# Optimization experiments

Measured on AMD Instinct MI355X. Metric: run time of the kernel, lower is better.

Reference implementation:

```python
import jax, jax.numpy as jnp
import numpy as np

NEG_INF = -9e15  # matches torch's -9000000000000000.0 fill
ALPHA = 0.2      # LeakyReLU negative slope


def setup_inputs() -> dict:
    key = jax.random.key(0)
    k1, k2, k3, k4 = jax.random.split(key, 4)
    B, F, N, T, C = 16, 128, 256, 64, 64
    h = jax.random.normal(k1, (B, F, N, T), dtype=jnp.float32)
    adj = jax.random.randint(k2, (B, N, N), 0, 2, dtype=jnp.int32)
    W = jax.random.normal(k3, (B, F, C), dtype=jnp.float32)
    a = jax.random.normal(k4, (B, 2 * C, 1), dtype=jnp.float32)
    return {"h": h, "adj": adj, "W": W, "a": a}


def reference(h, adj, W, a):
    # Wh: (B, C, N, T)
    Wh = jnp.einsum('bfnt,bfc->bcnt', h, W)
    C = W.shape[-1]
    # The original builds the O(N^2) pairwise concat then contracts with a.
    # Equivalently: e[b,i,j,t] = leakyrelu(a1.Wh[:, i] + a2.Wh[:, j])
    a1 = a[:, :C, 0]   # (B, C)
    a2 = a[:, C:, 0]   # (B, C)
    f = jnp.einsum('bcnt,bc->bnt', Wh, a1)  # (B, N, T)
    g = jnp.einsum('bcnt,bc->bnt', Wh, a2)  # (B, N, T)
    e = jax.nn.leaky_relu(f[:, :, None, :] + g[:, None, :, :], negative_slope=ALPHA)  # (B,N,N,T)
    mask = adj[:, :, :, None] > 0  # (B, N, N, 1) broadcast over T
    e = jnp.where(mask, e, NEG_INF)
    attention = jax.nn.softmax(e, axis=2)  # softmax over neighbor index m
    # dropout = 0.0 (eval-mode reference), so skipped
    h_prime = jnp.einsum('bnmt,bcmt->bcnt', attention, Wh)
    return jax.nn.elu(h_prime)  # concat=True branch
```

## Files before the change

### kernel.cpp

```cpp
#include <hip/hip_runtime.h>

#define B_ 16
#define F_ 128
#define N_ 256
#define T_ 64
#define C_ 64
#define ALPHA_ 0.2f
#define L2E_ 1.4426950408889634f

typedef short bf16x8 __attribute__((ext_vector_type(8)));
typedef float f32x4 __attribute__((ext_vector_type(4)));

__device__ __forceinline__ unsigned short f2bf(float x){
  unsigned int u = __float_as_uint(x);
  unsigned int r = u + 0x7FFFu + ((u >> 16) & 1u);
  return (unsigned short)(r >> 16);
}
__device__ __forceinline__ unsigned pk2(float a, float b){
  return ((unsigned)f2bf(b) << 16) | (unsigned)f2bf(a);
}
__device__ __forceinline__ unsigned sbit(unsigned w, int j){
  return (unsigned)(((int)(w << (31 - j))) >> 31);
}
__device__ __forceinline__ int swzT(int c){
  return ((c & 7) ^ ((c >> 3) & 7)) << 4;
}

__global__ void k_u(const float* __restrict__ W, const float* __restrict__ a,
                    float* __restrict__ u){
  int b = blockIdx.x, f = threadIdx.x;
  const float* Wb = W + (b*F_ + f)*C_;
  const float* ab = a + b*2*C_;
  float s1 = 0.f, s2 = 0.f;
#pragma unroll 8
  for (int c = 0; c < C_; ++c){
    float w = Wb[c];
    s1 = fmaf(w, ab[c], s1);
    s2 = fmaf(w, ab[C_ + c], s2);
  }
  u[b*F_ + f] = s1;
  u[B_*F_ + b*F_ + f] = s2;
}

__global__ void k_mask(const int* __restrict__ adj, unsigned* __restrict__ amask){
  int blk = blockIdx.x;
  int b = blk >> 2, r0 = (blk & 3)*64;
  int w = threadIdx.x >> 6, l = threadIdx.x & 63;
  const int* ab = adj + ((size_t)b*N_ + r0 + w*16)*N_;
  unsigned* om = amask + ((size_t)b*N_ + r0 + w*16)*8;
  for (int r = 0; r < 16; ++r){
    unsigned long long m0 = __ballot(ab[r*N_ +       l] > 0);
    unsigned long long m1 = __ballot(ab[r*N_ +  64 + l] > 0);
    unsigned long long m2 = __ballot(ab[r*N_ + 128 + l] > 0);
    unsigned long long m3 = __ballot(ab[r*N_ + 192 + l] > 0);
    if (l == 0){
      *(uint4*)(om + r*8)     = make_uint4((unsigned)m0, (unsigned)(m0>>32),
                                           (unsigned)m1, (unsigned)(m1>>32));
      *(uint4*)(om + r*8 + 4) = make_uint4((unsigned)m2, (unsigned)(m2>>32),
                                           (unsigned)m3, (unsigned)(m3>>32));
    }
  }
}

__global__ __launch_bounds__(256, 4) void k_wh(const float* __restrict__ h,
    const float* __restrict__ W, const float* __restrict__ u,
    unsigned short* __restrict__ wht, float* __restrict__ fvec,
    float* __restrict__ gvec){
  __shared__ uint4 hT4[1024];
  __shared__ uint4 wT4[1024];
  __shared__ float fpart[4][T_];
  __shared__ float gpart[4][T_];
  char* hT = (char*)hT4;
  char* wT = (char*)wT4;

  int bid = blockIdx.x, b = bid >> 8, n = bid & 255;
  int tid = threadIdx.x, w = tid >> 6, l = tid & 63;
  const float* hg = h + (size_t)b*F_*N_*T_ + n*T_;
  const float* Wg = W + b*F_*C_;
  const float* u1 = u + b*F_;
  const float* u2 = u + B_*F_ + b*F_;

  float sf = 0.f, sg = 0.f;
#pragma unroll
  for (int p = 0; p < 4; ++p){
    int f0 = p*32 + w*8;
    float v[8], wv[8];
#pragma unroll
    for (int j = 0; j < 8; ++j){
      v[j]  = hg[(size_t)(f0+j)*(N_*T_) + l];
      wv[j] = Wg[(f0+j)*C_ + l];
      sf = fmaf(v[j], u1[f0+j], sf);
      sg = fmaf(v[j], u2[f0+j], sg);
    }
    uint4 ph = make_uint4(pk2(v[0],v[1]),  pk2(v[2],v[3]),  pk2(v[4],v[5]),  pk2(v[6],v[7]));
    uint4 pw = make_uint4(pk2(wv[0],wv[1]),pk2(wv[2],wv[3]),pk2(wv[4],wv[5]),pk2(wv[6],wv[7]));
    *(uint4*)(hT + ((l*256 + f0*2) ^ ((l & 7) << 4))) = ph;
    *(uint4*)(wT + ((l*256 + f0*2) ^ ((l & 7) << 4))) = pw;
  }
  fpart[w][l] = sf;
  gpart[w][l] = sg;
  __syncthreads();

  if (tid < T_){
    float f_ = (fpart[0][tid] + fpart[1][tid]) + (fpart[2][tid] + fpart[3][tid]);
    float g_ = (gpart[0][tid] + gpart[1][tid]) + (gpart[2][tid] + gpart[3][tid]);
    fvec[(b*N_ + n)*T_ + tid] = f_ * L2E_;
    gvec[(b*N_ + n)*T_ + tid] = g_ * L2E_;
  }

  int li = l & 15, g_ = l >> 4;
  bf16x8 afr[4];
#pragma unroll
  for (int ch = 0; ch < 4; ++ch){
    int c = w*16 + li;
    afr[ch] = *(bf16x8*)(wT + ((c*256 + (ch*32 + g_*8)*2) ^ ((c & 7) << 4)));
  }
  f32x4 acc[4];
#pragma unroll
  for (int tt = 0; tt < 4; ++tt) acc[tt] = (f32x4){0.f,0.f,0.f,0.f};
#pragma unroll
  for (int tt = 0; tt < 4; ++tt){
#pragma unroll
    for (int ch = 0; ch < 4; ++ch){
      int t = tt*16 + li;
      bf16x8 bfr = *(bf16x8*)(hT + ((t*256 + (ch*32 + g_*8)*2) ^ ((t & 7) << 4)));
      acc[tt] = __builtin_amdgcn_mfma_f32_16x16x32_bf16(afr[ch], bfr, acc[tt], 0, 0, 0);
    }
  }
  unsigned short* wb = wht + ((size_t)b*T_*N_ + n)*C_;
#pragma unroll
  for (int tt = 0; tt < 4; ++tt){
    int t = tt*16 + li;
    int c0 = w*16 + g_*4;
    unsigned q0 = pk2(acc[tt][0], acc[tt][1]);
    unsigned q1 = pk2(acc[tt][2], acc[tt][3]);
    *(uint2*)(wb + (size_t)t*(N_*C_) + c0) = make_uint2(q0, q1);
  }
}

__global__ __launch_bounds__(256, 4) void k_attn(
    unsigned short* wht,
    const unsigned* __restrict__ amask,
    const float* __restrict__ fvec,
    const float* __restrict__ gvec){
  __shared__ uint4 whsT4[2048];
  __shared__ float gs[N_];
  __shared__ float fs[N_];
  __shared__ float invs[N_];
  char* dstT = (char*)whsT4;

  int bid = blockIdx.x;
  int b = bid >> 6, t = bid & 63;
  int tid = threadIdx.x, w = tid >> 6, l = tid & 63;
  int li = l & 15, g_ = l >> 4;

  gs[tid] = gvec[(b*N_ + tid)*T_ + t];
  fs[tid] = fvec[(b*N_ + tid)*T_ + t];

  uint4 mlo[4], mhi[4];
#pragma unroll
  for (int mt = 0; mt < 4; ++mt){
    int n = w*64 + mt*16 + li;
    const uint4* mp = (const uint4*)(amask + ((size_t)b*N_ + n)*8);
    mlo[mt] = mp[0];
    mhi[mt] = mp[1];
  }

  const char* src = (const char*)(wht + (size_t)(b*T_ + t)*(N_*C_));
#pragma unroll
  for (int i = 0; i < 4; ++i){
    int q2 = tid + i*256;
    int m = (q2 >> 3)*2, c0 = (q2 & 7)*8;
    uint4 ra = *(const uint4*)(src + m*128 + c0*2);
    uint4 rb = *(const uint4*)(src + (m+1)*128 + c0*2);
    unsigned va[4] = {ra.x, ra.y, ra.z, ra.w};
    unsigned vb[4] = {rb.x, rb.y, rb.z, rb.w};
#pragma unroll
    for (int k = 0; k < 4; ++k){
      int c = c0 + 2*k;
      unsigned lo = __builtin_amdgcn_perm(vb[k], va[k], 0x05040100u);
      unsigned hi = __builtin_amdgcn_perm(vb[k], va[k], 0x07060302u);
      *(unsigned*)(dstT + ((c*512 + m*2)     ^ swzT(c)))   = lo;
      *(unsigned*)(dstT + (((c+1)*512 + m*2) ^ swzT(c+1))) = hi;
    }
  }

  unsigned pkl[4], pkh[4];
  unsigned selA = 0x0C0C0000u | ((unsigned)(g_ + 4) << 8) | (unsigned)g_;
#pragma unroll
  for (int mt = 0; mt < 4; ++mt){
    unsigned t0 = __builtin_amdgcn_perm(mlo[mt].y, mlo[mt].x, selA);
    unsigned t1 = __builtin_amdgcn_perm(mlo[mt].w, mlo[mt].z, selA);
    pkl[mt] = __builtin_amdgcn_perm(t1, t0, 0x05040100u);
    unsigned t2 = __builtin_amdgcn_perm(mhi[mt].y, mhi[mt].x, selA);
    unsigned t3 = __builtin_amdgcn_perm(mhi[mt].w, mhi[mt].z, selA);
    pkh[mt] = __builtin_amdgcn_perm(t3, t2, 0x05040100u);
  }
  __syncthreads();

  float fl2[4];
#pragma unroll
  for (int mt = 0; mt < 4; ++mt) fl2[mt] = fs[w*64 + mt*16 + li];

  float mg[4] = {0.f, 0.f, 0.f, 0.f};
#pragma unroll 1
  for (int ch = 0; ch < 8; ++ch){
    const float* gq = &gs[ch*32 + g_*8];
    float4 ga = *(const float4*)gq;
    float4 gb = *(const float4*)(gq + 4);
    float gg[8] = {ga.x, ga.y, ga.z, ga.w, gb.x, gb.y, gb.z, gb.w};
    int sh = (ch & 3)*8;
#pragma unroll
    for (int mt = 0; mt < 4; ++mt){
      unsigned wsh = ((ch & 4) ? pkh[mt] : pkl[mt]) >> sh;
#pragma unroll
      for (int j = 0; j < 8; ++j){
        float cand = __uint_as_float(__float_as_uint(gg[j]) & sbit(wsh, j));
        mg[mt] = fmaxf(mg[mt], cand);
      }
    }
  }
  float fme[4], fme2[4];
#pragma unroll
  for (int mt = 0; mt < 4; ++mt){
    float v = mg[mt];
    v = fmaxf(v, __shfl_xor(v, 16));
    v = fmaxf(v, __shfl_xor(v, 32));
    float em = fl2[mt] + v;
    float M  = fmaxf(em, ALPHA_*em);
    fme[mt]  = fl2[mt] - M;
    fme2[mt] = fmaf(fl2[mt], ALPHA_, -M);
  }

  f32x4 acc[4][4];
#pragma unroll
  for (int mt = 0; mt < 4; ++mt)
#pragma unroll
    for (int nt = 0; nt < 4; ++nt)
      acc[mt][nt] = (f32x4){0.f, 0.f, 0.f, 0.f};
  float s0[4] = {0.f,0.f,0.f,0.f}, s1[4] = {0.f,0.f,0.f,0.f};

#pragma unroll 1
  for (int ch = 0; ch < 8; ++ch){
    bf16x8 bfr[4];
#pragma unroll
    for (int nt = 0; nt < 4; ++nt){
      int c = nt*16 + li;
      bfr[nt] = *(bf16x8*)(dstT + ((c*512 + (ch*32 + g_*8)*2) ^ swzT(c)));
    }
    const float* gq = &gs[ch*32 + g_*8];
    float4 ga = *(const float4*)gq;
    float4 gb = *(const float4*)(gq + 4);
    float gg[8] = {ga.x, ga.y, ga.z, ga.w, gb.x, gb.y, gb.z, gb.w};
    int sh = (ch & 3)*8;
#pragma unroll
    for (int mt = 0; mt < 4; ++mt){
      unsigned wsh = ((ch & 4) ? pkh[mt] : pkl[mt]) >> sh;
      float wv[8];
#pragma unroll
      for (int j = 0; j < 8; ++j){
        float d1 = gg[j] + fme[mt];
        float d2 = fmaf(gg[j], ALPHA_, fme2[mt]);
        float p  = exp2f(fmaxf(d1, d2));
        float v  = __uint_as_float(__float_as_uint(p) & sbit(wsh, j));
        if (j < 4) s0[mt] += v; else s1[mt] += v;
        wv[j] = v;
      }
      unsigned q0, q1, q2_, q3;
      asm("v_cvt_pk_bf16_f32 %0, %1, %2" : "=v"(q0)  : "v"(wv[0]), "v"(wv[1]));
      asm("v_cvt_pk_bf16_f32 %0, %1, %2" : "=v"(q1)  : "v"(wv[2]), "v"(wv[3]));
      asm("v_cvt_pk_bf16_f32 %0, %1, %2" : "=v"(q2_) : "v"(wv[4]), "v"(wv[5]));
      asm("v_cvt_pk_bf16_f32 %0, %1, %2" : "=v"(q3)  : "v"(wv[6]), "v"(wv[7]));
      union { unsigned u[4]; bf16x8 v; } afu;
      afu.u[0] = q0; afu.u[1] = q1; afu.u[2] = q2_; afu.u[3] = q3;
#pragma unroll
      for (int nt = 0; nt < 4; ++nt)
        acc[mt][nt] = __builtin_amdgcn_mfma_f32_16x16x32_bf16(afu.v, bfr[nt], acc[mt][nt], 0, 0, 0);
    }
  }

#pragma unroll
  for (int mt = 0; mt < 4; ++mt){
    float s = s0[mt] + s1[mt];
    s += __shfl_xor(s, 16);
    s += __shfl_xor(s, 32);
    if (g_ == 0) invs[w*64 + mt*16 + li] = 1.0f / s;
  }

  __syncthreads();
  char* outb = dstT;
#pragma unroll
  for (int mt = 0; mt < 4; ++mt){
#pragma unroll
    for (int reg = 0; reg < 4; ++reg){
      int nloc = w*64 + mt*16 + g_*4 + reg;
      float inv = invs[nloc];
#pragma unroll
      for (int nt = 0; nt < 4; ++nt){
        float v = acc[mt][nt][reg] * inv;
        v = v > 0.f ? v : (__expf(v) - 1.f);
        int c = nt*16 + li;
        int byteo = nloc*128 + (((c >> 3) ^ (nloc & 7)) << 4) + (c & 7)*2;
        *(unsigned short*)(outb + byteo) = f2bf(v);
      }
    }
  }
  __syncthreads();
  unsigned short* ob = wht + (size_t)(b*T_ + t)*(N_*C_);
#pragma unroll
  for (int k = 0; k < 8; ++k){
    int idx = tid + k*256;
    int nloc = idx >> 3, slot = idx & 7;
    uint4 vq = *(const uint4*)(outb + nloc*128 + ((slot ^ (nloc & 7)) << 4));
    *(uint4*)((char*)ob + (size_t)idx*16) = vq;
  }
}

__global__ __launch_bounds__(256) void k_tr(const unsigned short* __restrict__ whtO,
                                            float* __restrict__ out){
  __shared__ float tile[64][65];
  int bid = blockIdx.x;
  int b = bid >> 8, n = bid & 255;
  int tid = threadIdx.x;
  const unsigned short* src = whtO + ((size_t)b*T_*N_ + n)*C_;
#pragma unroll
  for (int i = 0; i < 2; ++i){
    int idx = tid + i*256;
    int t = idx >> 3, c0 = (idx & 7)*8;
    uint4 v = *(const uint4*)(src + (size_t)t*(N_*C_) + c0);
    unsigned arr[4] = {v.x, v.y, v.z, v.w};
#pragma unroll
    for (int k = 0; k < 4; ++k){
      tile[c0+2*k  ][t] = __uint_as_float(arr[k] << 16);
      tile[c0+2*k+1][t] = __uint_as_float(arr[k] & 0xFFFF0000u);
    }
  }
  __syncthreads();
  float* ob = out + (size_t)b*C_*N_*T_ + n*T_;
#pragma unroll
  for (int i = 0; i < 4; ++i){
    int idx = tid + i*256;
    int c = idx >> 4, t0 = (idx & 15)*4;
    float4 v = make_float4(tile[c][t0], tile[c][t0+1], tile[c][t0+2], tile[c][t0+3]);
    *(float4*)(ob + (size_t)c*(N_*T_) + t0) = v;
  }
}

extern "C" void kernel_launch(void* const* d_in, const int* in_sizes, int n_in,
                              void* d_out, int out_size, void* d_ws, size_t ws_size,
                              hipStream_t stream){
  (void)in_sizes; (void)n_in; (void)out_size; (void)ws_size;
  const float* h   = (const float*)d_in[0];
  const int*   adj = (const int*)d_in[1];
  const float* W   = (const float*)d_in[2];
  const float* a   = (const float*)d_in[3];
  float* u    = (float*)d_ws;
  float* fvec = u + 2*B_*F_;
  float* gvec = fvec + B_*N_*T_;
  unsigned short* wht = (unsigned short*)(gvec + B_*N_*T_);
  unsigned* amask = (unsigned*)(wht + (size_t)B_*T_*N_*C_);

  k_u   <<<dim3(B_),      dim3(F_),  0, stream>>>(W, a, u);
  k_mask<<<dim3(B_*4),    dim3(256), 0, stream>>>(adj, amask);
  k_wh  <<<dim3(B_*N_),   dim3(256), 0, stream>>>(h, W, u, wht, fvec, gvec);
  k_attn<<<dim3(B_*T_),   dim3(256), 0, stream>>>(wht, amask, fvec, gvec);
  k_tr  <<<dim3(B_*N_),   dim3(256), 0, stream>>>(wht, (float*)d_out);
}
```

Baseline: 114.5 us.

## Merge mask kernel into Wh kernel and overlap Wh tile loads with max pass

The adjacency-to-bitmask work now runs as extra blocks appended to the Wh projection kernel, which removes one kernel launch. In the attention kernel, the global loads of the transposed Wh tile are issued before the masked-max pass, and the transpose into shared memory happens after it, so load latency overlaps with that compute. The cost is higher register pressure from holding eight uint4 values across the max loop, plus a hand-placed barrier and waitcnt sequence that the shared-memory ordering now depends on.

```diff
diff --git a/kernel.cpp b/kernel.cpp
--- a/kernel.cpp
+++ b/kernel.cpp
@@ -42,30 +42,11 @@
   u[B_*F_ + b*F_ + f] = s2;
 }
 
-__global__ void k_mask(const int* __restrict__ adj, unsigned* __restrict__ amask){
-  int blk = blockIdx.x;
-  int b = blk >> 2, r0 = (blk & 3)*64;
-  int w = threadIdx.x >> 6, l = threadIdx.x & 63;
-  const int* ab = adj + ((size_t)b*N_ + r0 + w*16)*N_;
-  unsigned* om = amask + ((size_t)b*N_ + r0 + w*16)*8;
-  for (int r = 0; r < 16; ++r){
-    unsigned long long m0 = __ballot(ab[r*N_ +       l] > 0);
-    unsigned long long m1 = __ballot(ab[r*N_ +  64 + l] > 0);
-    unsigned long long m2 = __ballot(ab[r*N_ + 128 + l] > 0);
-    unsigned long long m3 = __ballot(ab[r*N_ + 192 + l] > 0);
-    if (l == 0){
-      *(uint4*)(om + r*8)     = make_uint4((unsigned)m0, (unsigned)(m0>>32),
-                                           (unsigned)m1, (unsigned)(m1>>32));
-      *(uint4*)(om + r*8 + 4) = make_uint4((unsigned)m2, (unsigned)(m2>>32),
-                                           (unsigned)m3, (unsigned)(m3>>32));
-    }
-  }
-}
-
-__global__ __launch_bounds__(256, 4) void k_wh(const float* __restrict__ h,
+__global__ __launch_bounds__(256, 4) void k_whm(const float* __restrict__ h,
     const float* __restrict__ W, const float* __restrict__ u,
+    const int* __restrict__ adj,
     unsigned short* __restrict__ wht, float* __restrict__ fvec,
-    float* __restrict__ gvec){
+    float* __restrict__ gvec, unsigned* __restrict__ amask){
   __shared__ uint4 hT4[1024];
   __shared__ uint4 wT4[1024];
   __shared__ float fpart[4][T_];
@@ -73,8 +54,30 @@
   char* hT = (char*)hT4;
   char* wT = (char*)wT4;
 
-  int bid = blockIdx.x, b = bid >> 8, n = bid & 255;
+  int bid = blockIdx.x;
   int tid = threadIdx.x, w = tid >> 6, l = tid & 63;
+
+  if (bid >= B_*N_){
+    int blk = bid - B_*N_;
+    int b = blk >> 2, r0 = (blk & 3)*64;
+    const int* ab = adj + ((size_t)b*N_ + r0 + w*16)*N_;
+    unsigned* om = amask + ((size_t)b*N_ + r0 + w*16)*8;
+    for (int r = 0; r < 16; ++r){
+      unsigned long long m0 = __ballot(ab[r*N_ +       l] > 0);
+      unsigned long long m1 = __ballot(ab[r*N_ +  64 + l] > 0);
+      unsigned long long m2 = __ballot(ab[r*N_ + 128 + l] > 0);
+      unsigned long long m3 = __ballot(ab[r*N_ + 192 + l] > 0);
+      if (l == 0){
+        *(uint4*)(om + r*8)     = make_uint4((unsigned)m0, (unsigned)(m0>>32),
+                                             (unsigned)m1, (unsigned)(m1>>32));
+        *(uint4*)(om + r*8 + 4) = make_uint4((unsigned)m2, (unsigned)(m2>>32),
+                                             (unsigned)m3, (unsigned)(m3>>32));
+      }
+    }
+    return;
+  }
+
+  int b = bid >> 8, n = bid & 255;
   const float* hg = h + (size_t)b*F_*N_*T_ + n*T_;
   const float* Wg = W + b*F_*C_;
   const float* u1 = u + b*F_;
@@ -165,26 +168,6 @@
     mlo[mt] = mp[0];
     mhi[mt] = mp[1];
   }
-
-  const char* src = (const char*)(wht + (size_t)(b*T_ + t)*(N_*C_));
-#pragma unroll
-  for (int i = 0; i < 4; ++i){
-    int q2 = tid + i*256;
-    int m = (q2 >> 3)*2, c0 = (q2 & 7)*8;
-    uint4 ra = *(const uint4*)(src + m*128 + c0*2);
-    uint4 rb = *(const uint4*)(src + (m+1)*128 + c0*2);
-    unsigned va[4] = {ra.x, ra.y, ra.z, ra.w};
-    unsigned vb[4] = {rb.x, rb.y, rb.z, rb.w};
-#pragma unroll
-    for (int k = 0; k < 4; ++k){
-      int c = c0 + 2*k;
-      unsigned lo = __builtin_amdgcn_perm(vb[k], va[k], 0x05040100u);
-      unsigned hi = __builtin_amdgcn_perm(vb[k], va[k], 0x07060302u);
-      *(unsigned*)(dstT + ((c*512 + m*2)     ^ swzT(c)))   = lo;
-      *(unsigned*)(dstT + (((c+1)*512 + m*2) ^ swzT(c+1))) = hi;
-    }
-  }
-
   unsigned pkl[4], pkh[4];
   unsigned selA = 0x0C0C0000u | ((unsigned)(g_ + 4) << 8) | (unsigned)g_;
 #pragma unroll
@@ -196,7 +179,20 @@
     unsigned t3 = __builtin_amdgcn_perm(mhi[mt].w, mhi[mt].z, selA);
     pkh[mt] = __builtin_amdgcn_perm(t3, t2, 0x05040100u);
   }
-  __syncthreads();
+
+  const char* src = (const char*)(wht + (size_t)(b*T_ + t)*(N_*C_));
+  uint4 ra[4], rb[4];
+#pragma unroll
+  for (int i = 0; i < 4; ++i){
+    int q2 = tid + i*256;
+    int m = (q2 >> 3)*2, c0 = (q2 & 7)*8;
+    ra[i] = *(const uint4*)(src + m*128 + c0*2);
+    rb[i] = *(const uint4*)(src + (m+1)*128 + c0*2);
+  }
+
+  asm volatile("s_waitcnt lgkmcnt(0)" ::: "memory");
+  __builtin_amdgcn_sched_barrier(0);
+  __builtin_amdgcn_s_barrier();
 
   float fl2[4];
 #pragma unroll
@@ -231,6 +227,23 @@
     fme[mt]  = fl2[mt] - M;
     fme2[mt] = fmaf(fl2[mt], ALPHA_, -M);
   }
+
+#pragma unroll
+  for (int i = 0; i < 4; ++i){
+    int q2 = tid + i*256;
+    int m = (q2 >> 3)*2, c0 = (q2 & 7)*8;
+    unsigned va[4] = {ra[i].x, ra[i].y, ra[i].z, ra[i].w};
+    unsigned vb[4] = {rb[i].x, rb[i].y, rb[i].z, rb[i].w};
+#pragma unroll
+    for (int k = 0; k < 4; ++k){
+      int c = c0 + 2*k;
+      unsigned lo = __builtin_amdgcn_perm(vb[k], va[k], 0x05040100u);
+      unsigned hi = __builtin_amdgcn_perm(vb[k], va[k], 0x07060302u);
+      *(unsigned*)(dstT + ((c*512 + m*2)     ^ swzT(c)))   = lo;
+      *(unsigned*)(dstT + (((c+1)*512 + m*2) ^ swzT(c+1))) = hi;
+    }
+  }
+  __syncthreads();
 
   f32x4 acc[4][4];
 #pragma unroll
@@ -360,9 +373,8 @@
   unsigned short* wht = (unsigned short*)(gvec + B_*N_*T_);
   unsigned* amask = (unsigned*)(wht + (size_t)B_*T_*N_*C_);
 
-  k_u   <<<dim3(B_),      dim3(F_),  0, stream>>>(W, a, u);
-  k_mask<<<dim3(B_*4),    dim3(256), 0, stream>>>(adj, amask);
-  k_wh  <<<dim3(B_*N_),   dim3(256), 0, stream>>>(h, W, u, wht, fvec, gvec);
-  k_attn<<<dim3(B_*T_),   dim3(256), 0, stream>>>(wht, amask, fvec, gvec);
-  k_tr  <<<dim3(B_*N_),   dim3(256), 0, stream>>>(wht, (float*)d_out);
-}
+  k_u   <<<dim3(B_),           dim3(F_),  0, stream>>>(W, a, u);
+  k_whm <<<dim3(B_*N_ + B_*4), dim3(256), 0, stream>>>(h, W, u, adj, wht, fvec, gvec, amask);
+  k_attn<<<dim3(B_*T_),        dim3(256), 0, stream>>>(wht, amask, fvec, gvec);
+  k_tr  <<<dim3(B_*N_),        dim3(256), 0, stream>>>(wht, (float*)d_out);
+}
```

Result: faster. 110.1 us (-3.8%).
